# Optimization experiments

Hardware: AMD Instinct MI355X
Metric: run time of the kernel (lower is better)

Reference implementation:

```python
import jax, jax.numpy as jnp
import numpy as np

# Conv2d_mvm config (matches init_kwargs): the bit-sliced crossbar MVM is a
# fixed-point emulation of an exact stride-1 conv2d with padding=1, no bias.
C_IN, C_OUT, K, H, W, PAD = 16, 16, 3, 1024, 1024, 1


def setup_inputs() -> dict:
    key = jax.random.key(0)
    kx, kw = jax.random.split(key)
    x = jax.random.normal(kx, (1, C_IN, H, W), dtype=jnp.float32)
    # kaiming_uniform-style init for the conv weight
    fan_in = C_IN * K * K
    bound = 1.0 / np.sqrt(fan_in)
    weight = jax.random.uniform(kw, (C_OUT, C_IN, K, K), dtype=jnp.float32,
                                minval=-bound, maxval=bound)
    return {"x": x, "weight": weight}


def reference(x, weight):
    # Ideal math of the bit-sliced crossbar MVM: per output pixel, the
    # flattened (C_in*K*K) receptive field dotted with each flattened filter.
    out = jax.lax.conv_general_dilated(
        x, weight,
        window_strides=(1, 1),
        padding=((PAD, PAD), (PAD, PAD)),
        dimension_numbers=("NCHW", "OIHW", "NCHW"),
    )
    # Original forward returns (C_out, H_out, W_out) with batch=1 assumed.
    return out[0]
```

## Files before the change

kernel.cpp:

```cpp
#include <hip/hip_runtime.h>


#define H 1024
#define W 1024
#define HW (H * W)
#define TW 64
#define TH 16
#define LPITCH 2112
#define LDS_BYTES 38016

typedef __bf16 bf16x8 __attribute__((ext_vector_type(8)));
typedef float f32x4 __attribute__((ext_vector_type(4)));
typedef unsigned short ushort8 __attribute__((ext_vector_type(8)));

__device__ __host__ inline unsigned short f2bf(float f) {
  unsigned u = __builtin_bit_cast(unsigned, f);
  return (unsigned short)((u + 0x7fffu + ((u >> 16) & 1u)) >> 16);
}

__global__ __launch_bounds__(256) void conv_prep(const float* __restrict__ w,
                                                 unsigned short* __restrict__ wA) {
  int i = blockIdx.x * 256 + threadIdx.x;
  if (i >= 5 * 64 * 8) return;
  int j = i & 7;
  int l = (i >> 3) & 63;
  int p = i >> 9;
  int k = (l >> 4) * 8 + j;
  int t = 2 * p + (k >> 4);
  int ci = k & 15;
  int co = l & 15;
  float v = (t <= 8) ? w[co * 144 + ci * 9 + t] : 0.f;
  wA[i] = f2bf(v);
}

__global__ __launch_bounds__(256, 4) void conv_mfma(
    const float* __restrict__ x, const unsigned short* __restrict__ wA,
    float* __restrict__ out) {
  __shared__ __align__(16) char lds[LDS_BYTES];

  const int tid  = threadIdx.x;
  const int lane = tid & 63;
  const int wave = tid >> 6;
  const int m = lane & 15;
  const int q = lane >> 4;
  const int colbase = blockIdx.x * TW;
  const int rowbase = blockIdx.y * TH;

  ushort8 aU[5];
#pragma unroll
  for (int p = 0; p < 5; ++p)
    aU[p] = *(const ushort8*)&wA[(p * 64 + lane) * 8];

  {
    const int rowx = rowbase - 1, colx = colbase - 1;
#pragma unroll
    for (int p2 = 0; p2 < 8; ++p2) {
      const float* xp0 = x + (2 * p2) * HW;
      const float* xp1 = xp0 + HW;
      for (int idx = tid; idx < 18 * 66; idx += 256) {
        int ly = idx / 66;
        int lx = idx - ly * 66;
        int gy = rowx + ly, gx = colx + lx;
        float v0 = 0.f, v1 = 0.f;
        if ((unsigned)gy < (unsigned)H && (unsigned)gx < (unsigned)W) {
          int o = gy * W + gx;
          v0 = xp0[o];
          v1 = xp1[o];
        }
        unsigned pk = (unsigned)f2bf(v0) | ((unsigned)f2bf(v1) << 16);
        int byte = ly * LPITCH + lx * 32 + p2 * 4;
        byte ^= ((lx >> 2) & 3) << 4;
        *(unsigned*)(lds + byte) = pk;
      }
    }
  }

  int baseaddr[5];
#pragma unroll
  for (int p = 0; p < 5; ++p) {
    int t = 2 * p + (q >> 1);
    int ky = 0, kx = 0;
    if (t <= 8) { ky = t / 3; kx = t - ky * 3; }
    int col = m + kx;
    int b = ky * LPITCH + col * 32 + (q & 1) * 16;
    b ^= ((col >> 2) & 3) << 4;
    baseaddr[p] = b + wave * 4 * LPITCH;
  }

  __syncthreads();

#pragma unroll
  for (int r = 0; r < 4; ++r) {
#pragma unroll
    for (int g = 0; g < 4; ++g) {
      f32x4 acc = {0.f, 0.f, 0.f, 0.f};
#pragma unroll
      for (int p = 0; p < 5; ++p) {
        ushort8 bU = *(const ushort8*)(lds + (baseaddr[p] + r * LPITCH + g * 512));
        acc = __builtin_amdgcn_mfma_f32_16x16x32_bf16(
            __builtin_bit_cast(bf16x8, aU[p]),
            __builtin_bit_cast(bf16x8, bU), acc, 0, 0, 0);
      }
      const int y  = rowbase + wave * 4 + r;
      const int x0 = colbase + g * 16 + m;
      float* op = out + y * W + x0;
#pragma unroll
      for (int j = 0; j < 4; ++j)
        op[(q * 4 + j) * HW] = acc[j];
    }
  }
}

extern "C" void kernel_launch(void* const* d_in, const int* in_sizes, int n_in,
                              void* d_out, int out_size, void* d_ws, size_t ws_size,
                              hipStream_t stream) {
  const float* x = (const float*)d_in[0];
  const float* w = (const float*)d_in[1];
  float* out = (float*)d_out;
  unsigned short* wA = (unsigned short*)d_ws;

  conv_prep<<<10, 256, 0, stream>>>(w, wA);

  dim3 grid(W / TW, H / TH);
  conv_mfma<<<grid, 256, 0, stream>>>(x, wA, out);
}
```

Baseline: 41.14 us.

## Vectorize halo loads, swap MFMA operands for float4 stores, halve tile height

The input halo fill now has each of 180 threads load float4 chunks from 8 channels at once, with clamped addresses and a mask multiply for zero padding. Each thread then writes 16-byte packed bf16 stores to LDS, replacing the old scalar per-element loop. The MFMA operands are swapped so each lane holds 4 consecutive output columns of one channel, which allows a single float4 global store instead of four strided scalar stores. Tile height drops from 16 to 8 rows and occupancy is raised to 5 blocks, trading more halo overhead for smaller LDS use and more blocks in flight.

```diff
diff --git a/kernel.cpp b/kernel.cpp
--- a/kernel.cpp
+++ b/kernel.cpp
@@ -5,13 +5,15 @@
 #define W 1024
 #define HW (H * W)
 #define TW 64
-#define TH 16
+#define TH 8
+#define LROWS 10
 #define LPITCH 2112
-#define LDS_BYTES 38016
+#define LDS_BYTES (LROWS * LPITCH)
 
 typedef __bf16 bf16x8 __attribute__((ext_vector_type(8)));
 typedef float f32x4 __attribute__((ext_vector_type(4)));
 typedef unsigned short ushort8 __attribute__((ext_vector_type(8)));
+typedef unsigned int uint4v __attribute__((ext_vector_type(4)));
 
 __device__ __host__ inline unsigned short f2bf(float f) {
   unsigned u = __builtin_bit_cast(unsigned, f);
@@ -33,7 +35,7 @@
   wA[i] = f2bf(v);
 }
 
-__global__ __launch_bounds__(256, 4) void conv_mfma(
+__global__ __launch_bounds__(256, 5) void conv_mfma(
     const float* __restrict__ x, const unsigned short* __restrict__ wA,
     float* __restrict__ out) {
   __shared__ __align__(16) char lds[LDS_BYTES];
@@ -46,34 +48,55 @@
   const int colbase = blockIdx.x * TW;
   const int rowbase = blockIdx.y * TH;
 
-  ushort8 aU[5];
+  if (tid < 180) {
+    const int ly  = tid / 18;
+    const int qx  = tid - ly * 18;
+    const int gy  = rowbase - 1 + ly;
+    const int gx0 = colbase - 4 + 4 * qx;
+    const bool rowok = (unsigned)gy < (unsigned)H;
+    const int gyc  = gy < 0 ? 0 : (gy > H - 1 ? H - 1 : gy);
+    const int gx0c = gx0 < 0 ? 0 : (gx0 > W - 4 ? W - 4 : gx0);
+    const float* xb = x + gyc * W + gx0c;
+
+    float fm[4];
+    int lok[4];
+    int lb[4];
+    int swz[4];
 #pragma unroll
-  for (int p = 0; p < 5; ++p)
-    aU[p] = *(const ushort8*)&wA[(p * 64 + lane) * 8];
-
-  {
-    const int rowx = rowbase - 1, colx = colbase - 1;
+    for (int i = 0; i < 4; ++i) {
+      const int gx = gx0 + i;
+      fm[i] = (rowok && (unsigned)gx < (unsigned)W) ? 1.f : 0.f;
+      const int lx = gx - (colbase - 1);
+      lok[i] = (unsigned)lx < 66u;
+      lb[i]  = ly * LPITCH + lx * 32;
+      swz[i] = ((lx >> 2) & 3) << 4;
+    }
 #pragma unroll
-    for (int p2 = 0; p2 < 8; ++p2) {
-      const float* xp0 = x + (2 * p2) * HW;
-      const float* xp1 = xp0 + HW;
-      for (int idx = tid; idx < 18 * 66; idx += 256) {
-        int ly = idx / 66;
-        int lx = idx - ly * 66;
-        int gy = rowx + ly, gx = colx + lx;
-        float v0 = 0.f, v1 = 0.f;
-        if ((unsigned)gy < (unsigned)H && (unsigned)gx < (unsigned)W) {
-          int o = gy * W + gx;
-          v0 = xp0[o];
-          v1 = xp1[o];
+    for (int h = 0; h < 2; ++h) {
+      f32x4 L[8];
+#pragma unroll
+      for (int c = 0; c < 8; ++c)
+        L[c] = *(const f32x4*)(xb + (h * 8 + c) * HW);
+#pragma unroll
+      for (int i = 0; i < 4; ++i) {
+        if (lok[i]) {
+          uint4v d;
+#pragma unroll
+          for (int p = 0; p < 4; ++p) {
+            const unsigned lo = f2bf(L[2 * p][i] * fm[i]);
+            const unsigned hi = f2bf(L[2 * p + 1][i] * fm[i]);
+            d[p] = lo | (hi << 16);
+          }
+          *(uint4v*)(lds + ((lb[i] + h * 16) ^ swz[i])) = d;
         }
-        unsigned pk = (unsigned)f2bf(v0) | ((unsigned)f2bf(v1) << 16);
-        int byte = ly * LPITCH + lx * 32 + p2 * 4;
-        byte ^= ((lx >> 2) & 3) << 4;
-        *(unsigned*)(lds + byte) = pk;
       }
     }
   }
+
+  ushort8 wU[5];
+#pragma unroll
+  for (int p = 0; p < 5; ++p)
+    wU[p] = *(const ushort8*)&wA[(p * 64 + lane) * 8];
 
   int baseaddr[5];
 #pragma unroll
@@ -84,13 +107,13 @@
     int col = m + kx;
     int b = ky * LPITCH + col * 32 + (q & 1) * 16;
     b ^= ((col >> 2) & 3) << 4;
-    baseaddr[p] = b + wave * 4 * LPITCH;
+    baseaddr[p] = b + wave * 2 * LPITCH;
   }
 
   __syncthreads();
 
 #pragma unroll
-  for (int r = 0; r < 4; ++r) {
+  for (int r = 0; r < 2; ++r) {
 #pragma unroll
     for (int g = 0; g < 4; ++g) {
       f32x4 acc = {0.f, 0.f, 0.f, 0.f};
@@ -98,15 +121,13 @@
       for (int p = 0; p < 5; ++p) {
         ushort8 bU = *(const ushort8*)(lds + (baseaddr[p] + r * LPITCH + g * 512));
         acc = __builtin_amdgcn_mfma_f32_16x16x32_bf16(
-            __builtin_bit_cast(bf16x8, aU[p]),
-            __builtin_bit_cast(bf16x8, bU), acc, 0, 0, 0);
+            __builtin_bit_cast(bf16x8, bU),
+            __builtin_bit_cast(bf16x8, wU[p]),
+            acc, 0, 0, 0);
       }
-      const int y  = rowbase + wave * 4 + r;
-      const int x0 = colbase + g * 16 + m;
-      float* op = out + y * W + x0;
-#pragma unroll
-      for (int j = 0; j < 4; ++j)
-        op[(q * 4 + j) * HW] = acc[j];
+      const int y  = rowbase + wave * 2 + r;
+      const int x0 = colbase + g * 16 + q * 4;
+      *(f32x4*)(out + m * HW + y * W + x0) = acc;
     }
   }
 }
```

Result: slower. 43.19 us (+5.0%).

## Stream input rows through a 4-slot LDS ring with software-pipelined loads

Applied to the files above, without the earlier changes.

Replaces the 64x16 tile, which loaded an 18x66 halo once and then computed, with 512-wide x 4-row strips. A rolling 4-row LDS ring buffer is filled with vectorized float4 global loads that are issued one row ahead of the MFMA compute. Blocks are mapped so each XCD handles a contiguous band of rows, and the MFMA operands are swapped so outputs are stored as float4 vectors. The goal is less halo overfetch and overlap of global load latency with compute, at the cost of more barriers, higher register pressure from 512-thread blocks, and only 512 blocks in the grid.

```diff
diff --git a/kernel.cpp b/kernel.cpp
--- a/kernel.cpp
+++ b/kernel.cpp
@@ -4,14 +4,19 @@
 #define H 1024
 #define W 1024
 #define HW (H * W)
-#define TW 64
-#define TH 16
-#define LPITCH 2112
-#define LDS_BYTES 38016
+#define TW 512
+#define RPB 4
+#define NQ 130
+#define NJ 260
+#define LCOLS 514
+#define PITCH (LCOLS * 32)
+#define NSLOT 4
+#define LDS_BYTES (NSLOT * PITCH)
 
 typedef __bf16 bf16x8 __attribute__((ext_vector_type(8)));
 typedef float f32x4 __attribute__((ext_vector_type(4)));
 typedef unsigned short ushort8 __attribute__((ext_vector_type(8)));
+typedef unsigned int uint4v __attribute__((ext_vector_type(4)));
 
 __device__ __host__ inline unsigned short f2bf(float f) {
   unsigned u = __builtin_bit_cast(unsigned, f);
@@ -33,7 +38,7 @@
   wA[i] = f2bf(v);
 }
 
-__global__ __launch_bounds__(256, 4) void conv_mfma(
+__global__ __launch_bounds__(512, 4) void conv_mfma(
     const float* __restrict__ x, const unsigned short* __restrict__ wA,
     float* __restrict__ out) {
   __shared__ __align__(16) char lds[LDS_BYTES];
@@ -43,72 +48,118 @@
   const int wave = tid >> 6;
   const int m = lane & 15;
   const int q = lane >> 4;
-  const int colbase = blockIdx.x * TW;
-  const int rowbase = blockIdx.y * TH;
 
-  ushort8 aU[5];
+  const int bid = blockIdx.x;
+  const int xcd = bid & 7;
+  const int u   = bid >> 3;
+  const int cb  = u & 1;
+  const int r0  = (xcd * 32 + (u >> 1)) * RPB;
+  const int colbase = cb * TW;
+
+  const bool st = tid < NJ;
+  int hf = 0, gx0 = 0;
+  const float* xcol = x;
+  if (st) {
+    hf  = tid & 1;
+    const int qx = tid >> 1;
+    gx0 = colbase - 4 + 4 * qx;
+    const int gx0c = gx0 < 0 ? 0 : (gx0 > W - 4 ? W - 4 : gx0);
+    xcol = x + hf * 8 * HW + gx0c;
+  }
+
+  f32x4 LA[8], LB[8];
+  float rmA, rmB;
+
+#define ISSUE(Lr, rm, y)                                                    \
+  {                                                                         \
+    const int gy = (y);                                                     \
+    rm = ((unsigned)gy < (unsigned)H) ? 1.f : 0.f;                          \
+    const int gyc = gy < 0 ? 0 : (gy > H - 1 ? H - 1 : gy);                 \
+    const float* xb = xcol + gyc * W;                                       \
+    if (st) {                                                               \
+      _Pragma("unroll") for (int c = 0; c < 8; ++c)                         \
+          Lr[c] = *(const f32x4*)(xb + c * HW);                             \
+    }                                                                       \
+  }
+
+#define PACK(Lr, rm, slot)                                                  \
+  if (st) {                                                                 \
+    char* const sb = lds + (slot) * PITCH;                                  \
+    _Pragma("unroll") for (int i = 0; i < 4; ++i) {                         \
+      const int gx = gx0 + i;                                               \
+      const int lx = gx - (colbase - 1);                                    \
+      if ((unsigned)lx < (unsigned)LCOLS) {                                 \
+        const float fm = rm * (((unsigned)gx < (unsigned)W) ? 1.f : 0.f);   \
+        uint4v d;                                                           \
+        _Pragma("unroll") for (int p = 0; p < 4; ++p) {                     \
+          const unsigned lo = f2bf(Lr[2 * p][i] * fm);                      \
+          const unsigned hi = f2bf(Lr[2 * p + 1][i] * fm);                  \
+          d[p] = lo | (hi << 16);                                           \
+        }                                                                   \
+        const int b = (lx * 32 + hf * 16) ^ (((lx >> 2) & 3) << 4);         \
+        *(uint4v*)(sb + b) = d;                                             \
+      }                                                                     \
+    }                                                                       \
+  }
+
+#define BAR()                                                \
+  asm volatile("s_waitcnt lgkmcnt(0)" ::: "memory");         \
+  asm volatile("s_barrier" ::: "memory")
+
+  ushort8 wU[5];
 #pragma unroll
   for (int p = 0; p < 5; ++p)
-    aU[p] = *(const ushort8*)&wA[(p * 64 + lane) * 8];
+    wU[p] = *(const ushort8*)&wA[(p * 64 + lane) * 8];
 
-  {
-    const int rowx = rowbase - 1, colx = colbase - 1;
-#pragma unroll
-    for (int p2 = 0; p2 < 8; ++p2) {
-      const float* xp0 = x + (2 * p2) * HW;
-      const float* xp1 = xp0 + HW;
-      for (int idx = tid; idx < 18 * 66; idx += 256) {
-        int ly = idx / 66;
-        int lx = idx - ly * 66;
-        int gy = rowx + ly, gx = colx + lx;
-        float v0 = 0.f, v1 = 0.f;
-        if ((unsigned)gy < (unsigned)H && (unsigned)gx < (unsigned)W) {
-          int o = gy * W + gx;
-          v0 = xp0[o];
-          v1 = xp1[o];
-        }
-        unsigned pk = (unsigned)f2bf(v0) | ((unsigned)f2bf(v1) << 16);
-        int byte = ly * LPITCH + lx * 32 + p2 * 4;
-        byte ^= ((lx >> 2) & 3) << 4;
-        *(unsigned*)(lds + byte) = pk;
-      }
-    }
-  }
-
-  int baseaddr[5];
+  int roff[5], kyv[5];
 #pragma unroll
   for (int p = 0; p < 5; ++p) {
     int t = 2 * p + (q >> 1);
     int ky = 0, kx = 0;
     if (t <= 8) { ky = t / 3; kx = t - ky * 3; }
-    int col = m + kx;
-    int b = ky * LPITCH + col * 32 + (q & 1) * 16;
-    b ^= ((col >> 2) & 3) << 4;
-    baseaddr[p] = b + wave * 4 * LPITCH;
+    const int col = m + kx;
+    roff[p] = (col * 32 + (q & 1) * 16) ^ (((col >> 2) & 3) << 4);
+    kyv[p] = ky;
   }
 
-  __syncthreads();
+#define COMPUTE(S)                                                          \
+  {                                                                         \
+    const int y = r0 + (S);                                                 \
+    float* const orow = out + m * HW + y * W + colbase + q * 4;             \
+    _Pragma("unroll") for (int gg = 0; gg < 4; ++gg) {                      \
+      f32x4 acc = {0.f, 0.f, 0.f, 0.f};                                     \
+      _Pragma("unroll") for (int p = 0; p < 5; ++p) {                       \
+        const int slot = ((S) + kyv[p]) & 3;                                \
+        const ushort8 bU = *(const ushort8*)(lds + slot * PITCH + roff[p] + \
+                                             (wave * 4 + gg) * 512);        \
+        acc = __builtin_amdgcn_mfma_f32_16x16x32_bf16(                      \
+            __builtin_bit_cast(bf16x8, bU),                \
+            __builtin_bit_cast(bf16x8, wU[p]),             \
+            acc, 0, 0, 0);                                                  \
+      }                                                                     \
+      *(f32x4*)(orow + (wave * 4 + gg) * 16) = acc;                         \
+    }                                                                       \
+  }
 
-#pragma unroll
-  for (int r = 0; r < 4; ++r) {
-#pragma unroll
-    for (int g = 0; g < 4; ++g) {
-      f32x4 acc = {0.f, 0.f, 0.f, 0.f};
-#pragma unroll
-      for (int p = 0; p < 5; ++p) {
-        ushort8 bU = *(const ushort8*)(lds + (baseaddr[p] + r * LPITCH + g * 512));
-        acc = __builtin_amdgcn_mfma_f32_16x16x32_bf16(
-            __builtin_bit_cast(bf16x8, aU[p]),
-            __builtin_bit_cast(bf16x8, bU), acc, 0, 0, 0);
-      }
-      const int y  = rowbase + wave * 4 + r;
-      const int x0 = colbase + g * 16 + m;
-      float* op = out + y * W + x0;
-#pragma unroll
-      for (int j = 0; j < 4; ++j)
-        op[(q * 4 + j) * HW] = acc[j];
-    }
-  }
+  ISSUE(LA, rmA, r0 - 1);
+  ISSUE(LB, rmB, r0);
+  PACK(LA, rmA, 0);
+  PACK(LB, rmB, 1);
+  ISSUE(LA, rmA, r0 + 1);
+
+  PACK(LA, rmA, 2); ISSUE(LB, rmB, r0 + 2);
+  BAR(); COMPUTE(0);
+  PACK(LB, rmB, 3); ISSUE(LA, rmA, r0 + 3);
+  BAR(); COMPUTE(1);
+  PACK(LA, rmA, 0); ISSUE(LB, rmB, r0 + 4);
+  BAR(); COMPUTE(2);
+  PACK(LB, rmB, 1);
+  BAR(); COMPUTE(3);
+
+#undef ISSUE
+#undef PACK
+#undef BAR
+#undef COMPUTE
 }
 
 extern "C" void kernel_launch(void* const* d_in, const int* in_sizes, int n_in,
@@ -121,6 +172,5 @@
 
   conv_prep<<<10, 256, 0, stream>>>(w, wA);
 
-  dim3 grid(W / TW, H / TH);
-  conv_mfma<<<grid, 256, 0, stream>>>(x, wA, out);
+  conv_mfma<<<dim3(512), 512, 0, stream>>>(x, wA, out);
 }
```

New measurement: 41.01 us. No clear change (-0.3%).
